# Kernel optimization log

Measured on AMD Instinct MI355X. Metric: run time of the kernel, lower is better.

## Reference

```python
import jax, jax.numpy as jnp
import numpy as np

N = 10000; E = 160000; NF = 5; EF = 3; H = 8; C = 128; HC = H * C; G = 16

def _glorot(key, shape):
    s = float(np.sqrt(6.0 / (shape[0] + shape[-1])))
    return jax.random.uniform(key, shape, minval=-s, maxval=s, dtype=jnp.float32)

def setup_inputs():
    key = jax.random.key(0)
    ks = jax.random.split(key, 32)
    inp = {}
    inp["x"] = jax.random.normal(ks[0], (N, NF), dtype=jnp.float32)
    inp["edge_index"] = jax.random.randint(ks[1], (2, E), 0, N, dtype=jnp.int32)
    inp["edge_attr"] = jax.random.normal(ks[2], (E, EF), dtype=jnp.float32)
    inp["batch"] = jnp.sort(jax.random.randint(ks[3], (N,), 0, G, dtype=jnp.int32))
    ins = [NF, HC, HC, HC]
    i = 4
    for l in range(4):
        inp[f"W{l+1}"] = _glorot(ks[i], (ins[l], HC)); i += 1
        inp[f"We{l+1}"] = _glorot(ks[i], (EF, HC)); i += 1
        inp[f"as{l+1}"] = _glorot(ks[i], (H, C)); i += 1
        inp[f"ad{l+1}"] = _glorot(ks[i], (H, C)); i += 1
        inp[f"ae{l+1}"] = _glorot(ks[i], (H, C)); i += 1
        inp[f"b{l+1}"] = jnp.zeros((HC if l < 3 else C,), jnp.float32)
    inp["lin_w"] = _glorot(ks[i], (C, 1)) * 2.0
    inp["lin_b"] = jnp.zeros((1,), jnp.float32)
    return inp

def _gat(x, src, dst, ea, W, We, a_s, a_d, a_e, bias, concat):
    # PyG GATConv with edge_dim, add_self_loops=True, fill_value='mean'
    n = x.shape[0]
    cnt = jax.ops.segment_sum(jnp.ones((src.shape[0],), x.dtype), dst, n)
    loop_attr = jax.ops.segment_sum(ea, dst, n) / jnp.maximum(cnt, 1.0)[:, None]
    sl = jnp.arange(n, dtype=src.dtype)
    src2 = jnp.concatenate([src, sl])
    dst2 = jnp.concatenate([dst, sl])
    ea2 = jnp.concatenate([ea, loop_attr], axis=0)
    xl = (x @ W).reshape(n, H, C)                       # [N,H,C]
    a_src = jnp.einsum("nhc,hc->nh", xl, a_s)
    a_dst = jnp.einsum("nhc,hc->nh", xl, a_d)
    el = (ea2 @ We).reshape(-1, H, C)                    # [E2,H,C]
    alpha = a_src[src2] + a_dst[dst2] + jnp.einsum("ehc,hc->eh", el, a_e)
    alpha = jax.nn.leaky_relu(alpha, 0.2)
    m = jax.ops.segment_max(alpha, dst2, n)
    m = jnp.where(jnp.isfinite(m), m, 0.0)
    ex = jnp.exp(alpha - m[dst2])
    den = jax.ops.segment_sum(ex, dst2, n)
    alpha = ex / (den[dst2] + 1e-16)                     # segment softmax over dst
    out = jax.ops.segment_sum(alpha[:, :, None] * xl[src2], dst2, n)  # [N,H,C]
    if concat:
        return out.reshape(n, HC) + bias
    return out.mean(axis=1) + bias

def reference(x, edge_index, edge_attr, batch,
              W1, We1, as1, ad1, ae1, b1,
              W2, We2, as2, ad2, ae2, b2,
              W3, We3, as3, ad3, ae3, b3,
              W4, We4, as4, ad4, ae4, b4,
              lin_w, lin_b):
    src, dst = edge_index[0], edge_index[1]
    h = jax.nn.elu(_gat(x, src, dst, edge_attr, W1, We1, as1, ad1, ae1, b1, True))
    h = jax.nn.elu(_gat(h, src, dst, edge_attr, W2, We2, as2, ad2, ae2, b2, True))
    h = jax.nn.elu(_gat(h, src, dst, edge_attr, W3, We3, as3, ad3, ae3, b3, True))
    h = jax.nn.elu(_gat(h, src, dst, edge_attr, W4, We4, as4, ad4, ae4, b4, False))
    cnt = jax.ops.segment_sum(jnp.ones((N,), h.dtype), batch, G)
    pooled = jax.ops.segment_sum(h, batch, G) / jnp.maximum(cnt, 1.0)[:, None]
    return (pooled @ lin_w + lin_b).squeeze(-1)
```

## Files before the change

### kernel.cpp

```cpp
#include <hip/hip_runtime.h>
#include <math.h>

#define Nn 10000
#define En 160000
#define NF 5
#define EF 3
#define Hh 8
#define Cc 128
#define HC 1024
#define Gg 16

#define Mpad 10112

typedef __attribute__((ext_vector_type(8))) _Float16 half8;
typedef __attribute__((ext_vector_type(4))) float f32x4;


__device__ __forceinline__ void gl_lds16(const void* g, void* l) {
    __builtin_amdgcn_global_load_lds((const __attribute__((address_space(1))) void*)g,
                                     (__attribute__((address_space(3))) void*)l, 16, 0, 0);
}

__device__ __forceinline__ float elu_f(float v) {
    return (v > 0.f) ? v : expm1f(v);
}


__global__ void deg_sum_k(const int* __restrict__ dst, const float* __restrict__ ea,
                          int* __restrict__ cnt, float* __restrict__ sum_ea) {
    int e = blockIdx.x * 256 + threadIdx.x;
    if (e >= En) return;
    int d = dst[e];
    atomicAdd(&cnt[d], 1);
    atomicAdd(&sum_ea[d * 3 + 0], ea[e * 3 + 0]);
    atomicAdd(&sum_ea[d * 3 + 1], ea[e * 3 + 1]);
    atomicAdd(&sum_ea[d * 3 + 2], ea[e * 3 + 2]);
}

__global__ void finish_loop_k(const int* __restrict__ cnt, float* __restrict__ loop_attr) {
    int n = blockIdx.x * 256 + threadIdx.x;
    if (n >= Nn) return;
    float s = 1.0f / fmaxf((float)cnt[n], 1.0f);
    loop_attr[n * 3 + 0] *= s;
    loop_attr[n * 3 + 1] *= s;
    loop_attr[n * 3 + 2] *= s;
}

__global__ __launch_bounds__(1024) void scan_k(const int* __restrict__ cnt,
                                               int* __restrict__ rowptr,
                                               int* __restrict__ fillptr) {
    __shared__ int sh[1024];
    int tid = threadIdx.x;
    int base = 0;
    for (int chunk = 0; chunk < Nn; chunk += 1024) {
        int i = chunk + tid;
        int v = (i < Nn) ? cnt[i] : 0;
        sh[tid] = v;
        __syncthreads();
        for (int off = 1; off < 1024; off <<= 1) {
            int t = (tid >= off) ? sh[tid - off] : 0;
            __syncthreads();
            sh[tid] += t;
            __syncthreads();
        }
        int excl = sh[tid] - v;
        if (i < Nn) { rowptr[i] = base + excl; fillptr[i] = base + excl; }
        int total = sh[1023];
        __syncthreads();
        base += total;
    }
    if (tid == 0) rowptr[Nn] = base;
}

__global__ void csr_fill_k(const int* __restrict__ src, const int* __restrict__ dst,
                           const float* __restrict__ ea, int* __restrict__ fillptr,
                           int* __restrict__ srcP, float4* __restrict__ eaP) {
    int e = blockIdx.x * 256 + threadIdx.x;
    if (e >= En) return;
    int d = dst[e];
    int pos = atomicAdd(&fillptr[d], 1);
    srcP[pos] = src[e];
    eaP[pos] = make_float4(ea[e * 3 + 0], ea[e * 3 + 1], ea[e * 3 + 2], 0.f);
}

__global__ void bounds_k(const int* __restrict__ batch, int* __restrict__ gstart) {
    int i = blockIdx.x * 256 + threadIdx.x;
    if (i >= Nn) return;
    int b = batch[i];
    if (i == 0) {
        for (int g = 0; g <= b; ++g) gstart[g] = 0;
    } else {
        int pb = batch[i - 1];
        for (int g = pb + 1; g <= b; ++g) gstart[g] = i;
    }
    if (i == Nn - 1) {
        for (int g = b + 1; g <= Gg; ++g) gstart[g] = Nn;
    }
}


__global__ void wae_all_k(const float* __restrict__ We1, const float* __restrict__ ae1,
                          const float* __restrict__ We2, const float* __restrict__ ae2,
                          const float* __restrict__ We3, const float* __restrict__ ae3,
                          const float* __restrict__ We4, const float* __restrict__ ae4,
                          float* __restrict__ w_ae_all) {
    int t = threadIdx.x;
    if (t >= 96) return;
    int l = t / 24, idx = t % 24;
    int f = idx >> 3, h = idx & 7;
    const float* We = (l == 0) ? We1 : (l == 1) ? We2 : (l == 2) ? We3 : We4;
    const float* ae = (l == 0) ? ae1 : (l == 1) ? ae2 : (l == 2) ? ae3 : ae4;
    float s = 0.f;
    for (int c = 0; c < Cc; ++c) s += We[f * HC + h * Cc + c] * ae[h * Cc + c];
    w_ae_all[l * 24 + f * 8 + h] = s;
}

__global__ __launch_bounds__(1024) void wsplit_all_k(const float* __restrict__ W2,
                                                     const float* __restrict__ W3,
                                                     const float* __restrict__ W4,
                                                     _Float16* __restrict__ Wt16) {
    __shared__ float tile[32][33];
    int z = blockIdx.z;
    const float* W = (z == 0) ? W2 : (z == 1) ? W3 : W4;
    int nb = blockIdx.x * 32, kb = blockIdx.y * 32;
    tile[threadIdx.y][threadIdx.x] = W[(size_t)(kb + threadIdx.y) * HC + nb + threadIdx.x];
    __syncthreads();
    float x = tile[threadIdx.x][threadIdx.y];
    int n = nb + threadIdx.y, k = kb + threadIdx.x;
    Wt16[(size_t)z * HC * HC + (size_t)n * HC + k] = (_Float16)x;
}


__global__ void gemm_k5(const float* __restrict__ x, const float* __restrict__ Wm,
                        const float* __restrict__ a_s, const float* __restrict__ a_d,
                        _Float16* __restrict__ out16,
                        float* __restrict__ a_srcB, float* __restrict__ a_dstB) {
    int n = blockIdx.x;
    int tid = threadIdx.x;
    __shared__ float xr[8];
    __shared__ float vrow[HC];
    if (tid < NF) xr[tid] = x[n * NF + tid];
    __syncthreads();
    float x0 = xr[0], x1 = xr[1], x2 = xr[2], x3 = xr[3], x4 = xr[4];
    for (int j = tid; j < HC; j += 256) {
        float v = x0 * Wm[j] + x1 * Wm[HC + j] + x2 * Wm[2 * HC + j]
                + x3 * Wm[3 * HC + j] + x4 * Wm[4 * HC + j];
        out16[(size_t)n * HC + j] = (_Float16)v;
        vrow[j] = v;
    }
    __syncthreads();
    int w = tid >> 6, lane = tid & 63;
#pragma unroll
    for (int q = 0; q < 2; ++q) {
        int h = w * 2 + q;
        float v0 = vrow[h * Cc + lane], v1 = vrow[h * Cc + 64 + lane];
        float s1 = v0 * a_s[h * Cc + lane] + v1 * a_s[h * Cc + 64 + lane];
        float s2 = v0 * a_d[h * Cc + lane] + v1 * a_d[h * Cc + 64 + lane];
#pragma unroll
        for (int off = 32; off; off >>= 1) {
            s1 += __shfl_xor(s1, off);
            s2 += __shfl_xor(s2, off);
        }
        if (lane == 0) { a_srcB[n * 8 + h] = s1; a_dstB[n * 8 + h] = s2; }
    }
}

__global__ __launch_bounds__(256) void gemm_mfma(const _Float16* __restrict__ A,
                                                 const _Float16* __restrict__ Bt,
                                                 const float* __restrict__ a_s,
                                                 const float* __restrict__ a_d,
                                                 _Float16* __restrict__ C16,
                                                 float* __restrict__ a_srcB,
                                                 float* __restrict__ a_dstB) {
    __shared__ _Float16 As[128 * 32];
    __shared__ _Float16 Bs[128 * 32];
    __shared__ float ps[128][2];
    __shared__ float pd[128][2];
    int tid = threadIdx.x;
    int wave = tid >> 6, lane = tid & 63;
    int wr = wave >> 1, wc = wave & 1;
    int row0 = blockIdx.y * 128;
    int col0 = blockIdx.x * 128;
    int h = blockIdx.x;

    f32x4 acc[4][4];
#pragma unroll
    for (int i = 0; i < 4; ++i)
#pragma unroll
        for (int j = 0; j < 4; ++j) acc[i][j] = (f32x4){0.f, 0.f, 0.f, 0.f};

    int srow = lane >> 2;
    int scol = (lane & 3) * 8;
    int fr = lane & 15;
    int fk = (lane >> 4) * 8;

    for (int kb = 0; kb < 1024; kb += 32) {
#pragma unroll
        for (int cc = 0; cc < 2; ++cc) {
            int c = wave + cc * 4;
            int r = c * 16 + srow;
            gl_lds16(A + (size_t)(row0 + r) * 1024 + kb + scol, &As[c * 512 + lane * 8]);
            gl_lds16(Bt + (size_t)(col0 + r) * 1024 + kb + scol, &Bs[c * 512 + lane * 8]);
        }
        __syncthreads();

        half8 af[4], bf[4];
#pragma unroll
        for (int i = 0; i < 4; ++i)
            af[i] = *(const half8*)&As[(wr * 64 + i * 16 + fr) * 32 + fk];
#pragma unroll
        for (int j = 0; j < 4; ++j)
            bf[j] = *(const half8*)&Bs[(wc * 64 + j * 16 + fr) * 32 + fk];
#pragma unroll
        for (int i = 0; i < 4; ++i)
#pragma unroll
            for (int j = 0; j < 4; ++j)
                acc[i][j] = __builtin_amdgcn_mfma_f32_16x16x32_f16(af[i], bf[j], acc[i][j],
                                                                   0, 0, 0);
        __syncthreads();
    }

    int cn = lane & 15, rq = (lane >> 4) * 4;
#pragma unroll
    for (int i = 0; i < 4; ++i) {
        int rbase = row0 + wr * 64 + i * 16 + rq;
#pragma unroll
        for (int j = 0; j < 4; ++j) {
            int col = col0 + wc * 64 + j * 16 + cn;
#pragma unroll
            for (int r = 0; r < 4; ++r) {
                int row = rbase + r;
                if (row < Nn) C16[(size_t)row * HC + col] = (_Float16)acc[i][j][r];
            }
        }
    }
    float asv[4], adv[4];
#pragma unroll
    for (int j = 0; j < 4; ++j) {
        int c = wc * 64 + j * 16 + cn;
        asv[j] = a_s[h * Cc + c];
        adv[j] = a_d[h * Cc + c];
    }
#pragma unroll
    for (int i = 0; i < 4; ++i)
#pragma unroll
        for (int r = 0; r < 4; ++r) {
            float rs = acc[i][0][r] * asv[0] + acc[i][1][r] * asv[1]
                     + acc[i][2][r] * asv[2] + acc[i][3][r] * asv[3];
            float rd = acc[i][0][r] * adv[0] + acc[i][1][r] * adv[1]
                     + acc[i][2][r] * adv[2] + acc[i][3][r] * adv[3];
#pragma unroll
            for (int off = 1; off < 16; off <<= 1) {
                rs += __shfl_xor(rs, off);
                rd += __shfl_xor(rd, off);
            }
            if (cn == 0) {
                int rib = wr * 64 + i * 16 + rq + r;
                ps[rib][wc] = rs;
                pd[rib][wc] = rd;
            }
        }
    __syncthreads();
    if (tid < 128) {
        int row = row0 + tid;
        if (row < Nn) {
            a_srcB[row * 8 + h] = ps[tid][0] + ps[tid][1];
            a_dstB[row * 8 + h] = pd[tid][0] + pd[tid][1];
        }
    }
}


__global__ __launch_bounds__(256) void aggregate_k(const _Float16* __restrict__ xl16,
                                                   const float4* __restrict__ eaP,
                                                   const float* __restrict__ loop_attr,
                                                   const float* __restrict__ a_srcB,
                                                   const float* __restrict__ a_dstB,
                                                   const float* __restrict__ w_ae,
                                                   const int* __restrict__ rowptr,
                                                   const int* __restrict__ srcP,
                                                   const float* __restrict__ bias,
                                                   const float* __restrict__ lin_w,
                                                   _Float16* __restrict__ A2,
                                                   float* __restrict__ dnode,
                                                   int raw_mode) {
    int n = (blockIdx.x * 256 + threadIdx.x) >> 6;
    int lane = threadIdx.x & 63;
    if (n >= Nn) return;
    int beg = rowptr[n], end = rowptr[n + 1];
    int hh = lane & 7;
    int slot = lane >> 3;
    int hc = lane >> 3;

    float w0 = w_ae[hh], w1 = w_ae[8 + hh], w2 = w_ae[16 + hh];
    float adst_n = a_dstB[n * 8 + hh];
    float asrc_n = a_srcB[n * 8 + hh];
    float f0 = loop_attr[n * 3 + 0], f1 = loop_attr[n * 3 + 1], f2 = loop_attr[n * 3 + 2];
    float av = asrc_n + adst_n + f0 * w0 + f1 * w1 + f2 * w2;
    float aself = (av > 0.f) ? av : 0.2f * av;

    float m = (slot == 0) ? aself : -3.0e38f;
    float s = (slot == 0) ? 1.0f : 0.0f;
    for (int i = beg + slot; i < end; i += 8) {
        int sn = srcP[i];
        float4 e4 = eaP[i];
        float a = a_srcB[sn * 8 + hh] + adst_n + e4.x * w0 + e4.y * w1 + e4.z * w2;
        a = (a > 0.f) ? a : 0.2f * a;
        if (a > m) { s = s * __expf(m - a) + 1.0f; m = a; }
        else s += __expf(a - m);
    }
#pragma unroll
    for (int off = 8; off < 64; off <<= 1) {
        float mo = __shfl_xor(m, off);
        float so = __shfl_xor(s, off);
        float M = fmaxf(m, mo);
        s = s * __expf(m - M) + so * __expf(mo - M);
        m = M;
    }
    float inv = 1.f / (s + 1e-16f);
    float wself = __expf(aself - m) * inv;

    float m_c = __shfl(m, hc);
    float inv_c = __shfl(inv, hc);
    float wself_c = __shfl(wself, hc);
    float adst_nc = __shfl(adst_n, hc);
    float w0c = w_ae[hc], w1c = w_ae[8 + hc], w2c = w_ae[16 + hc];

    float acc[16];
    {
        const _Float16* r = xl16 + (size_t)n * HC + lane * 16;
        half8 r0 = *(const half8*)r;
        half8 r1 = *(const half8*)(r + 8);
#pragma unroll
        for (int j = 0; j < 8; ++j) {
            acc[j] = wself_c * (float)r0[j];
            acc[8 + j] = wself_c * (float)r1[j];
        }
    }
    int loff = lane * 16;
    for (int i0 = beg; i0 < end; i0 += 4) {
        int last = end - 1;
        bool v1 = (i0 + 1 < end), v2 = (i0 + 2 < end), v3 = (i0 + 3 < end);
        int i1 = v1 ? i0 + 1 : last;
        int i2 = v2 ? i0 + 2 : last;
        int i3 = v3 ? i0 + 3 : last;
        int s0 = srcP[i0], s1 = srcP[i1], s2 = srcP[i2], s3 = srcP[i3];
        float4 e0 = eaP[i0], e1 = eaP[i1], e2 = eaP[i2], e3 = eaP[i3];
        float as0 = a_srcB[s0 * 8 + hc], as1 = a_srcB[s1 * 8 + hc];
        float as2 = a_srcB[s2 * 8 + hc], as3 = a_srcB[s3 * 8 + hc];
        const _Float16* p0 = xl16 + (size_t)s0 * HC + loff;
        const _Float16* p1 = xl16 + (size_t)s1 * HC + loff;
        const _Float16* p2 = xl16 + (size_t)s2 * HC + loff;
        const _Float16* p3 = xl16 + (size_t)s3 * HC + loff;
        half8 q0a = *(const half8*)p0, q0b = *(const half8*)(p0 + 8);
        half8 q1a = *(const half8*)p1, q1b = *(const half8*)(p1 + 8);
        half8 q2a = *(const half8*)p2, q2b = *(const half8*)(p2 + 8);
        half8 q3a = *(const half8*)p3, q3b = *(const half8*)(p3 + 8);
        float al0 = as0 + adst_nc + e0.x * w0c + e0.y * w1c + e0.z * w2c;
        float al1 = as1 + adst_nc + e1.x * w0c + e1.y * w1c + e1.z * w2c;
        float al2 = as2 + adst_nc + e2.x * w0c + e2.y * w1c + e2.z * w2c;
        float al3 = as3 + adst_nc + e3.x * w0c + e3.y * w1c + e3.z * w2c;
        al0 = (al0 > 0.f) ? al0 : 0.2f * al0;
        al1 = v1 ? ((al1 > 0.f) ? al1 : 0.2f * al1) : -3.0e38f;
        al2 = v2 ? ((al2 > 0.f) ? al2 : 0.2f * al2) : -3.0e38f;
        al3 = v3 ? ((al3 > 0.f) ? al3 : 0.2f * al3) : -3.0e38f;
        float u0 = __expf(al0 - m_c) * inv_c;
        float u1 = __expf(al1 - m_c) * inv_c;
        float u2 = __expf(al2 - m_c) * inv_c;
        float u3 = __expf(al3 - m_c) * inv_c;
#pragma unroll
        for (int j = 0; j < 8; ++j) {
            float t0 = acc[j], t1 = acc[8 + j];
            t0 = fmaf(u0, (float)q0a[j], t0);  t1 = fmaf(u0, (float)q0b[j], t1);
            t0 = fmaf(u1, (float)q1a[j], t0);  t1 = fmaf(u1, (float)q1b[j], t1);
            t0 = fmaf(u2, (float)q2a[j], t0);  t1 = fmaf(u2, (float)q2b[j], t1);
            t0 = fmaf(u3, (float)q3a[j], t0);  t1 = fmaf(u3, (float)q3b[j], t1);
            acc[j] = t0; acc[8 + j] = t1;
        }
    }

    if (!raw_mode) {
        int ch = lane * 16;
        half8 hv0, hv1;
#pragma unroll
        for (int j = 0; j < 8; ++j) {
            hv0[j] = (_Float16)elu_f(acc[j] + bias[ch + j]);
            hv1[j] = (_Float16)elu_f(acc[8 + j] + bias[ch + 8 + j]);
        }
        _Float16* p = A2 + (size_t)n * 1024 + ch;
        *(half8*)p = hv0;
        *(half8*)(p + 8) = hv1;
    } else {
#pragma unroll
        for (int off = 8; off < 64; off <<= 1)
#pragma unroll
            for (int j = 0; j < 16; ++j) acc[j] += __shfl_xor(acc[j], off);
        int c0 = (lane & 7) * 16;
        float partial = 0.f;
#pragma unroll
        for (int j = 0; j < 16; ++j) {
            float v = elu_f(acc[j] * 0.125f + bias[c0 + j]);
            partial = fmaf(v, lin_w[c0 + j], partial);
        }
#pragma unroll
        for (int off = 1; off < 8; off <<= 1) partial += __shfl_xor(partial, off);
        if (lane == 0) dnode[n] = partial;
    }
}


__global__ __launch_bounds__(256) void pool_final_k(const float* __restrict__ dnode,
                                                    const int* __restrict__ gstart,
                                                    const float* __restrict__ lin_b,
                                                    float* __restrict__ out) {
    __shared__ float sh[256];
    int g = blockIdx.x;
    int tid = threadIdx.x;
    int s = gstart[g], e = gstart[g + 1];
    float acc = 0.f;
    for (int n = s + tid; n < e; n += 256) acc += dnode[n];
    sh[tid] = acc;
    __syncthreads();
    for (int off = 128; off; off >>= 1) {
        if (tid < off) sh[tid] += sh[tid + off];
        __syncthreads();
    }
    if (tid == 0) out[g] = sh[0] / fmaxf((float)(e - s), 1.f) + lin_b[0];
}


extern "C" void kernel_launch(void* const* d_in, const int* in_sizes, int n_in,
                              void* d_out, int out_size, void* d_ws, size_t ws_size,
                              hipStream_t stream) {
    const float* x = (const float*)d_in[0];
    const int* ei = (const int*)d_in[1];
    const float* ea = (const float*)d_in[2];
    const int* batch = (const int*)d_in[3];
    const float *Wl[4], *Wel[4], *asl[4], *adl[4], *ael[4], *bl[4];
    for (int l = 0; l < 4; ++l) {
        Wl[l] = (const float*)d_in[4 + 6 * l];
        Wel[l] = (const float*)d_in[5 + 6 * l];
        asl[l] = (const float*)d_in[6 + 6 * l];
        adl[l] = (const float*)d_in[7 + 6 * l];
        ael[l] = (const float*)d_in[8 + 6 * l];
        bl[l] = (const float*)d_in[9 + 6 * l];
    }
    const float* lin_w = (const float*)d_in[28];
    const float* lin_b = (const float*)d_in[29];
    const int* srcA = ei;
    const int* dstA = ei + En;

    float* Wp = (float*)d_ws;
    size_t o = 0;
    _Float16* A2 = (_Float16*)(Wp + o); o += (size_t)Mpad * 512;
    _Float16* Wt16 = (_Float16*)(Wp + o); o += (size_t)3 * HC * HC / 2;
    _Float16* xl16 = (_Float16*)(Wp + o); o += (size_t)Nn * HC / 2;
    float4* eaP = (float4*)(Wp + o); o += (size_t)En * 4;
    float* loop_attr = Wp + o; o += Nn * 3;
    int* cnt = (int*)(Wp + o); o += Nn;
    int* rowptr = (int*)(Wp + o); o += Nn + 1;
    int* fillptr = (int*)(Wp + o); o += Nn;
    int* srcP = (int*)(Wp + o); o += En;
    int* gstart = (int*)(Wp + o); o += Gg + 1;
    float* a_srcB = Wp + o; o += Nn * Hh;
    float* a_dstB = Wp + o; o += Nn * Hh;
    float* w_ae_all = Wp + o; o += 128;
    float* dnode = Wp + o; o += Nn;

    hipMemsetAsync(cnt, 0, Nn * sizeof(int), stream);
    hipMemsetAsync(loop_attr, 0, Nn * 3 * sizeof(float), stream);

    deg_sum_k<<<(En + 255) / 256, 256, 0, stream>>>(dstA, ea, cnt, loop_attr);
    finish_loop_k<<<(Nn + 255) / 256, 256, 0, stream>>>(cnt, loop_attr);
    scan_k<<<1, 1024, 0, stream>>>(cnt, rowptr, fillptr);
    csr_fill_k<<<(En + 255) / 256, 256, 0, stream>>>(srcA, dstA, ea, fillptr, srcP, eaP);
    bounds_k<<<(Nn + 255) / 256, 256, 0, stream>>>(batch, gstart);
    wae_all_k<<<1, 128, 0, stream>>>(Wel[0], ael[0], Wel[1], ael[1], Wel[2], ael[2],
                                     Wel[3], ael[3], w_ae_all);
    wsplit_all_k<<<dim3(32, 32, 3), dim3(32, 32), 0, stream>>>(Wl[1], Wl[2], Wl[3], Wt16);

    for (int l = 0; l < 4; ++l) {
        if (l == 0)
            gemm_k5<<<Nn, 256, 0, stream>>>(x, Wl[0], asl[0], adl[0], xl16, a_srcB, a_dstB);
        else
            gemm_mfma<<<dim3(HC / 128, Mpad / 128), 256, 0, stream>>>(
                A2, Wt16 + (size_t)(l - 1) * HC * HC, asl[l], adl[l], xl16, a_srcB, a_dstB);
        aggregate_k<<<(Nn + 3) / 4, 256, 0, stream>>>(xl16, eaP, loop_attr, a_srcB,
                                                      a_dstB, w_ae_all + l * 24, rowptr,
                                                      srcP, bl[l], lin_w, A2, dnode,
                                                      (l == 3) ? 1 : 0);
    }
    pool_final_k<<<Gg, 256, 0, stream>>>(dnode, gstart, lin_b, (float*)d_out);
}
```

Before: 599.0 us.

## Fuse preprocessing kernels into single-pass scan and reorder GEMM LDS layout

The loop-attr normalization and graph-boundary kernels are folded into the scan kernel. The scan itself becomes one pass in which each thread owns ten elements, replacing the ten chunked block scans. The MFMA GEMM also changes how it stages tiles in LDS: each lane loads a k-quarter of a row, and fragments are read in that k-quarter-major layout. That layout is likely meant to cut LDS bank conflicts on fragment reads. The aim is fewer launches, fewer barriers, and cheaper LDS access, but the single-block scan now does more serial work per thread.

```diff
diff --git a/kernel.cpp b/kernel.cpp
--- a/kernel.cpp
+++ b/kernel.cpp
@@ -37,39 +37,65 @@
     atomicAdd(&sum_ea[d * 3 + 2], ea[e * 3 + 2]);
 }
 
-__global__ void finish_loop_k(const int* __restrict__ cnt, float* __restrict__ loop_attr) {
-    int n = blockIdx.x * 256 + threadIdx.x;
-    if (n >= Nn) return;
-    float s = 1.0f / fmaxf((float)cnt[n], 1.0f);
-    loop_attr[n * 3 + 0] *= s;
-    loop_attr[n * 3 + 1] *= s;
-    loop_attr[n * 3 + 2] *= s;
-}
-
 __global__ __launch_bounds__(1024) void scan_k(const int* __restrict__ cnt,
                                                int* __restrict__ rowptr,
-                                               int* __restrict__ fillptr) {
+                                               int* __restrict__ fillptr,
+                                               float* __restrict__ loop_attr,
+                                               const int* __restrict__ batch,
+                                               int* __restrict__ gstart) {
     __shared__ int sh[1024];
     int tid = threadIdx.x;
-    int base = 0;
-    for (int chunk = 0; chunk < Nn; chunk += 1024) {
-        int i = chunk + tid;
-        int v = (i < Nn) ? cnt[i] : 0;
-        sh[tid] = v;
+    int base = tid * 10;
+    int loc[10];
+    int tsum = 0;
+#pragma unroll
+    for (int j = 0; j < 10; ++j) {
+        int i = base + j;
+        int v = 0;
+        if (i < Nn) {
+            v = cnt[i];
+            float s = 1.0f / fmaxf((float)v, 1.0f);
+            loop_attr[i * 3 + 0] *= s;
+            loop_attr[i * 3 + 1] *= s;
+            loop_attr[i * 3 + 2] *= s;
+        }
+        loc[j] = tsum;
+        tsum += v;
+    }
+    sh[tid] = tsum;
+    __syncthreads();
+    for (int off = 1; off < 1024; off <<= 1) {
+        int t = (tid >= off) ? sh[tid - off] : 0;
         __syncthreads();
-        for (int off = 1; off < 1024; off <<= 1) {
-            int t = (tid >= off) ? sh[tid - off] : 0;
-            __syncthreads();
-            sh[tid] += t;
-            __syncthreads();
-        }
-        int excl = sh[tid] - v;
-        if (i < Nn) { rowptr[i] = base + excl; fillptr[i] = base + excl; }
-        int total = sh[1023];
+        sh[tid] += t;
         __syncthreads();
-        base += total;
-    }
-    if (tid == 0) rowptr[Nn] = base;
+    }
+    int excl = sh[tid] - tsum;
+#pragma unroll
+    for (int j = 0; j < 10; ++j) {
+        int i = base + j;
+        if (i < Nn) {
+            rowptr[i] = excl + loc[j];
+            fillptr[i] = excl + loc[j];
+        }
+    }
+    if (tid == 1023) rowptr[Nn] = sh[1023];
+#pragma unroll
+    for (int j = 0; j < 10; ++j) {
+        int i = base + j;
+        if (i < Nn) {
+            int b = batch[i];
+            if (i == 0) {
+                for (int g = 0; g <= b; ++g) gstart[g] = 0;
+            } else {
+                int pb = batch[i - 1];
+                for (int g = pb + 1; g <= b; ++g) gstart[g] = i;
+            }
+            if (i == Nn - 1) {
+                for (int g = b + 1; g <= Gg; ++g) gstart[g] = Nn;
+            }
+        }
+    }
 }
 
 __global__ void csr_fill_k(const int* __restrict__ src, const int* __restrict__ dst,
@@ -81,21 +107,6 @@
     int pos = atomicAdd(&fillptr[d], 1);
     srcP[pos] = src[e];
     eaP[pos] = make_float4(ea[e * 3 + 0], ea[e * 3 + 1], ea[e * 3 + 2], 0.f);
-}
-
-__global__ void bounds_k(const int* __restrict__ batch, int* __restrict__ gstart) {
-    int i = blockIdx.x * 256 + threadIdx.x;
-    if (i >= Nn) return;
-    int b = batch[i];
-    if (i == 0) {
-        for (int g = 0; g <= b; ++g) gstart[g] = 0;
-    } else {
-        int pb = batch[i - 1];
-        for (int g = pb + 1; g <= b; ++g) gstart[g] = i;
-    }
-    if (i == Nn - 1) {
-        for (int g = b + 1; g <= Gg; ++g) gstart[g] = Nn;
-    }
 }
 
 
@@ -189,28 +200,28 @@
 #pragma unroll
         for (int j = 0; j < 4; ++j) acc[i][j] = (f32x4){0.f, 0.f, 0.f, 0.f};
 
-    int srow = lane >> 2;
-    int scol = (lane & 3) * 8;
+    int srow = lane & 15;
+    int skq = (lane >> 4) * 8;
     int fr = lane & 15;
-    int fk = (lane >> 4) * 8;
+    int kq = lane >> 4;
 
     for (int kb = 0; kb < 1024; kb += 32) {
 #pragma unroll
         for (int cc = 0; cc < 2; ++cc) {
             int c = wave + cc * 4;
             int r = c * 16 + srow;
-            gl_lds16(A + (size_t)(row0 + r) * 1024 + kb + scol, &As[c * 512 + lane * 8]);
-            gl_lds16(Bt + (size_t)(col0 + r) * 1024 + kb + scol, &Bs[c * 512 + lane * 8]);
+            gl_lds16(A + (size_t)(row0 + r) * 1024 + kb + skq, &As[c * 512 + lane * 8]);
+            gl_lds16(Bt + (size_t)(col0 + r) * 1024 + kb + skq, &Bs[c * 512 + lane * 8]);
         }
         __syncthreads();
 
         half8 af[4], bf[4];
 #pragma unroll
         for (int i = 0; i < 4; ++i)
-            af[i] = *(const half8*)&As[(wr * 64 + i * 16 + fr) * 32 + fk];
+            af[i] = *(const half8*)&As[(wr * 4 + i) * 512 + kq * 128 + fr * 8];
 #pragma unroll
         for (int j = 0; j < 4; ++j)
-            bf[j] = *(const half8*)&Bs[(wc * 64 + j * 16 + fr) * 32 + fk];
+            bf[j] = *(const half8*)&Bs[(wc * 4 + j) * 512 + kq * 128 + fr * 8];
 #pragma unroll
         for (int i = 0; i < 4; ++i)
 #pragma unroll
@@ -471,10 +482,8 @@
     hipMemsetAsync(loop_attr, 0, Nn * 3 * sizeof(float), stream);
 
     deg_sum_k<<<(En + 255) / 256, 256, 0, stream>>>(dstA, ea, cnt, loop_attr);
-    finish_loop_k<<<(Nn + 255) / 256, 256, 0, stream>>>(cnt, loop_attr);
-    scan_k<<<1, 1024, 0, stream>>>(cnt, rowptr, fillptr);
+    scan_k<<<1, 1024, 0, stream>>>(cnt, rowptr, fillptr, loop_attr, batch, gstart);
     csr_fill_k<<<(En + 255) / 256, 256, 0, stream>>>(srcA, dstA, ea, fillptr, srcP, eaP);
-    bounds_k<<<(Nn + 255) / 256, 256, 0, stream>>>(batch, gstart);
     wae_all_k<<<1, 128, 0, stream>>>(Wel[0], ael[0], Wel[1], ael[1], Wel[2], ael[2],
                                      Wel[3], ael[3], w_ae_all);
     wsplit_all_k<<<dim3(32, 32, 3), dim3(32, 32), 0, stream>>>(Wl[1], Wl[2], Wl[3], Wt16);
```

Result: slower. 647.6 us (+8.1%).
